# Kernel tuning notes

Hardware: AMD Instinct MI355X
Metric: run time of the kernel (lower is better)

Reference implementation:

```python
import jax, jax.numpy as jnp
import numpy as np

N_NODES = 50000
N_EDGES = 800000
D_IN = 128
D_HID = 128
NUM_LAYERS = 3
NUM_GRAPHS = 50


def setup_inputs() -> dict:
    key = jax.random.key(0)
    ks = jax.random.split(key, 8)
    x = jax.random.normal(ks[0], (N_NODES, D_IN), dtype=jnp.float32)
    edge_index = jax.random.randint(ks[1], (2, N_EDGES), 0, N_NODES, dtype=jnp.int32)
    batch = jnp.sort(jax.random.randint(ks[2], (N_NODES,), 0, NUM_GRAPHS, dtype=jnp.int32))
    # glorot-ish init for GCN weights and fc weights
    scale = 1.0 / np.sqrt(D_HID)
    Wc = jax.random.normal(ks[3], (NUM_LAYERS, D_IN, D_HID), dtype=jnp.float32) * scale
    bc = jnp.zeros((NUM_LAYERS, D_HID), dtype=jnp.float32)
    Wf = jax.random.normal(ks[4], (NUM_LAYERS, D_HID, D_HID), dtype=jnp.float32) * scale
    bf = jnp.zeros((NUM_LAYERS, D_HID), dtype=jnp.float32)
    return {"x": x, "edge_index": edge_index, "batch": batch,
            "Wc": Wc, "bc": bc, "Wf": Wf, "bf": bf}


def _gcn_forward(x, Wc, bc, Wf, bf, src, dst, deg_inv_sqrt, batch):
    norm = deg_inv_sqrt[src] * deg_inv_sqrt[dst]  # [E+N]
    for i in range(NUM_LAYERS):
        h = x @ Wc[i]                              # [N, D_HID] linear transform
        msg = h[src] * norm[:, None]               # gather + normalize, [E+N, D_HID]
        x = jax.ops.segment_sum(msg, dst, num_segments=N_NODES) + bc[i]
        x = jax.nn.relu(x)
    x = jax.ops.segment_sum(x, batch, num_segments=NUM_GRAPHS)  # global_add_pool
    for i in range(NUM_LAYERS):
        x = jax.nn.relu(x @ Wf[i] + bf[i])
    return x  # [NUM_GRAPHS, D_HID]


def reference(x, edge_index, batch, Wc, bc, Wf, bf):
    # add self-loops (PyG GCNConv default) and compute symmetric normalization
    loops = jnp.arange(N_NODES, dtype=edge_index.dtype)
    src = jnp.concatenate([edge_index[0], loops])
    dst = jnp.concatenate([edge_index[1], loops])
    deg = jax.ops.segment_sum(jnp.ones_like(dst, dtype=x.dtype), dst,
                              num_segments=N_NODES)
    deg_inv_sqrt = jnp.where(deg > 0, jax.lax.rsqrt(jnp.maximum(deg, 1.0)), 0.0)
    return _gcn_forward(x, Wc, bc, Wf, bf, src, dst, deg_inv_sqrt, batch)
```

## Files before the change

kernel.cpp:

```cpp
#include <hip/hip_runtime.h>

#define N_NODES 50000
#define N_EDGES 800000
#define D 128
#define NGRAPH 50

typedef unsigned int uint32;
typedef unsigned short u16;
typedef __attribute__((ext_vector_type(8))) short short8;
typedef __attribute__((ext_vector_type(4))) float f32x4;

__device__ inline float bf_lo(uint32 u) { union { uint32 u; float f; } c; c.u = u << 16; return c.f; }
__device__ inline float bf_hi(uint32 u) { union { uint32 u; float f; } c; c.u = u & 0xffff0000u; return c.f; }
__device__ inline u16 f2bf(float f) {
  union { float f; uint32 u; } c; c.f = f;
  uint32 r = (c.u + 0x7fffu + ((c.u >> 16) & 1u)) >> 16;
  return (u16)r;
}

__global__ void k_init(int* __restrict__ deg, const float* __restrict__ Wc,
                       u16* __restrict__ WT, const int* __restrict__ batch,
                       int* __restrict__ gstart) {
  int i = blockIdx.x * 256 + threadIdx.x;
  if (i < N_NODES) deg[i] = 0;
  if (i < 3 * 128 * 128) {
    int layer = i >> 14, rem = i & 16383;
    int n = rem >> 7, k = rem & 127;
    WT[i] = f2bf(Wc[layer * 16384 + k * 128 + n]);
  }
  if (i <= NGRAPH) {
    int lo = 0, hi = N_NODES;
    while (lo < hi) {
      int mid = (lo + hi) >> 1;
      if (batch[mid] < i) lo = mid + 1; else hi = mid;
    }
    gstart[i] = lo;
  }
}

__global__ void k_degfill(const int* __restrict__ src, const int* __restrict__ dst,
                          int* __restrict__ deg, u16* __restrict__ csr) {
  int e = blockIdx.x * 256 + threadIdx.x;
  if (e < N_EDGES) {
    int d = dst[e];
    int r = atomicAdd(&deg[d], 1);
    csr[(d << 6) + r] = (u16)src[e];
  }
}

template <int AF32>
__global__ __launch_bounds__(256) void k_gemm(const void* __restrict__ Ap,
                                              const u16* __restrict__ WT,
                                              const int* __restrict__ deg,
                                              u16* __restrict__ G) {
  __shared__ u16 so[4][16][136];
  int t = threadIdx.x;
  int wave = t >> 6, l = t & 63;
  int cl = l & 15, kgrp = l >> 4;
  int r0 = blockIdx.x * 64 + wave * 16;
  int arow = r0 + cl;
  bool valid = arow < N_NODES;

  const short8* B8 = reinterpret_cast<const short8*>(WT);

  f32x4 acc[8] = {};
#pragma unroll
  for (int k0 = 0; k0 < 4; ++k0) {
    short8 a = {};
    if (valid) {
      if (AF32) {
        const float4* A4 = reinterpret_cast<const float4*>(Ap);
        float4 v0 = A4[(size_t)arow * 32 + (k0 * 4 + kgrp) * 2];
        float4 v1 = A4[(size_t)arow * 32 + (k0 * 4 + kgrp) * 2 + 1];
        a[0] = (short)f2bf(v0.x); a[1] = (short)f2bf(v0.y);
        a[2] = (short)f2bf(v0.z); a[3] = (short)f2bf(v0.w);
        a[4] = (short)f2bf(v1.x); a[5] = (short)f2bf(v1.y);
        a[6] = (short)f2bf(v1.z); a[7] = (short)f2bf(v1.w);
      } else {
        a = reinterpret_cast<const short8*>(Ap)[(size_t)arow * 16 + k0 * 4 + kgrp];
      }
    }
#pragma unroll
    for (int c = 0; c < 8; ++c) {
      short8 b = B8[(c * 16 + cl) * 16 + k0 * 4 + kgrp];
      acc[c] = __builtin_amdgcn_mfma_f32_16x16x32_bf16(a, b, acc[c], 0, 0, 0);
    }
  }

  int rloc = kgrp * 4;
  float dj[4];
#pragma unroll
  for (int j = 0; j < 4; ++j) {
    int rr = r0 + rloc + j;
    dj[j] = (rr < N_NODES) ? rsqrtf((float)deg[rr] + 1.0f) : 0.f;
  }
#pragma unroll
  for (int c = 0; c < 8; ++c) {
#pragma unroll
    for (int j = 0; j < 4; ++j) {
      so[wave][rloc + j][c * 16 + cl] = f2bf(dj[j] * acc[c][j]);
    }
  }
#pragma unroll
  for (int i = 0; i < 4; ++i) {
    int idx = i * 64 + l;
    int rr = idx >> 4, ch = idx & 15;
    int grow = r0 + rr;
    if (grow < N_NODES) {
      *reinterpret_cast<uint4*>(&(((u16*)G)[(size_t)grow * 128 + ch * 8])) =
          *reinterpret_cast<const uint4*>(&so[wave][rr][ch * 8]);
    }
  }
}

template <int OUT_BF16>
__global__ __launch_bounds__(256) void k_agg(const uint2* __restrict__ g2,
                                             const int* __restrict__ deg,
                                             const u16* __restrict__ csr,
                                             const float* __restrict__ bc,
                                             void* __restrict__ xo) {
  int w = threadIdx.x >> 6;
  int i = blockIdx.x * 4 + w;
  if (i >= N_NODES) return;
  int l = threadIdx.x & 63;
  int half = l >> 5, c = l & 31;

  int cnt = deg[i];
  float di = rsqrtf((float)cnt + 1.0f);

  float a0 = 0.f, a1 = 0.f, a2 = 0.f, a3 = 0.f;
  if (half == 0) {
    uint2 su = g2[(size_t)i * 32 + c];
    a0 = bf_lo(su.x); a1 = bf_hi(su.x); a2 = bf_lo(su.y); a3 = bf_hi(su.y);
  }

  int myidx = (l < cnt) ? (int)csr[(i << 6) + l] : 0;
  int npair = cnt >> 1;
  int j = 0;
  for (; j + 4 <= npair; j += 4) {
    int s0 = __shfl(myidx, 2 * j + half);
    int s1 = __shfl(myidx, 2 * (j + 1) + half);
    int s2 = __shfl(myidx, 2 * (j + 2) + half);
    int s3 = __shfl(myidx, 2 * (j + 3) + half);
    uint2 u0 = g2[(size_t)s0 * 32 + c];
    uint2 u1 = g2[(size_t)s1 * 32 + c];
    uint2 u2 = g2[(size_t)s2 * 32 + c];
    uint2 u3 = g2[(size_t)s3 * 32 + c];
    a0 += bf_lo(u0.x); a1 += bf_hi(u0.x); a2 += bf_lo(u0.y); a3 += bf_hi(u0.y);
    a0 += bf_lo(u1.x); a1 += bf_hi(u1.x); a2 += bf_lo(u1.y); a3 += bf_hi(u1.y);
    a0 += bf_lo(u2.x); a1 += bf_hi(u2.x); a2 += bf_lo(u2.y); a3 += bf_hi(u2.y);
    a0 += bf_lo(u3.x); a1 += bf_hi(u3.x); a2 += bf_lo(u3.y); a3 += bf_hi(u3.y);
  }
  for (; j < npair; ++j) {
    int s = __shfl(myidx, 2 * j + half);
    uint2 u = g2[(size_t)s * 32 + c];
    a0 += bf_lo(u.x); a1 += bf_hi(u.x); a2 += bf_lo(u.y); a3 += bf_hi(u.y);
  }
  if (cnt & 1) {
    int s = __shfl(myidx, cnt - 1);
    if (half == 0) {
      uint2 u = g2[(size_t)s * 32 + c];
      a0 += bf_lo(u.x); a1 += bf_hi(u.x); a2 += bf_lo(u.y); a3 += bf_hi(u.y);
    }
  }
  a0 += __shfl_xor(a0, 32);
  a1 += __shfl_xor(a1, 32);
  a2 += __shfl_xor(a2, 32);
  a3 += __shfl_xor(a3, 32);

  if (half == 0) {
    float4 bb = reinterpret_cast<const float4*>(bc)[c];
    float r0 = fmaxf(fmaf(di, a0, bb.x), 0.f);
    float r1 = fmaxf(fmaf(di, a1, bb.y), 0.f);
    float r2 = fmaxf(fmaf(di, a2, bb.z), 0.f);
    float r3 = fmaxf(fmaf(di, a3, bb.w), 0.f);
    if (OUT_BF16) {
      ushort4 o;
      o.x = f2bf(r0); o.y = f2bf(r1); o.z = f2bf(r2); o.w = f2bf(r3);
      reinterpret_cast<ushort4*>(xo)[(size_t)i * 32 + c] = o;
    } else {
      reinterpret_cast<float4*>(xo)[(size_t)i * 32 + c] = make_float4(r0, r1, r2, r3);
    }
  }
}

__global__ __launch_bounds__(256) void k_pool(const float* __restrict__ x,
                                              const int* __restrict__ gstart,
                                              float* __restrict__ pp) {
  __shared__ float2 red[4][64];
  int g = blockIdx.x, ch = blockIdx.y;
  int s = gstart[g], e = gstart[g + 1];
  long len = e - s;
  int cs = s + (int)(len * ch / 8);
  int ce = s + (int)(len * (ch + 1) / 8);
  int sub = threadIdx.x >> 6, l = threadIdx.x & 63;
  const float2* x2 = reinterpret_cast<const float2*>(x);
  float2 acc = make_float2(0.f, 0.f);
  for (int n = cs + sub; n < ce; n += 4) {
    float2 v = x2[(size_t)n * 64 + l];
    acc.x += v.x;
    acc.y += v.y;
  }
  red[sub][l] = acc;
  __syncthreads();
  if (sub == 0) {
    float2 a = red[0][l];
    a.x += red[1][l].x + red[2][l].x + red[3][l].x;
    a.y += red[1][l].y + red[2][l].y + red[3][l].y;
    pp[(ch * NGRAPH + g) * D + 2 * l] = a.x;
    pp[(ch * NGRAPH + g) * D + 2 * l + 1] = a.y;
  }
}

__global__ __launch_bounds__(128) void k_fc(const float* __restrict__ pp,
                                            const float* __restrict__ Wf,
                                            const float* __restrict__ bf,
                                            float* __restrict__ out) {
  __shared__ float row[D];
  int g = blockIdx.x, c = threadIdx.x;
  float v = 0.f;
#pragma unroll
  for (int ch = 0; ch < 8; ++ch) v += pp[(ch * NGRAPH + g) * D + c];
  row[c] = v;
  __syncthreads();
  for (int l = 0; l < 3; ++l) {
    const float* W = Wf + l * D * D;
    float s = bf[l * D + c];
    for (int k = 0; k < D; ++k) s = fmaf(row[k], W[k * D + c], s);
    s = fmaxf(s, 0.f);
    __syncthreads();
    row[c] = s;
    __syncthreads();
  }
  out[g * D + c] = row[c];
}

extern "C" void kernel_launch(void* const* d_in, const int* in_sizes, int n_in,
                              void* d_out, int out_size, void* d_ws, size_t ws_size,
                              hipStream_t stream) {
  const float* x   = (const float*)d_in[0];
  const int*   ei  = (const int*)d_in[1];
  const int* batch = (const int*)d_in[2];
  const float* Wc  = (const float*)d_in[3];
  const float* bc  = (const float*)d_in[4];
  const float* Wf  = (const float*)d_in[5];
  const float* bf  = (const float*)d_in[6];
  float* out = (float*)d_out;
  const int* src = ei;
  const int* dst = ei + N_EDGES;

  char* ws = (char*)d_ws;
  size_t o = 0;
  auto take = [&](size_t b) -> void* {
    void* p = ws + o;
    o = (o + b + 255) & ~(size_t)255;
    return p;
  };
  int*  deg    = (int*)take(N_NODES * 4);
  int*  gstart = (int*)take(64 * 4);
  u16*  WT     = (u16*)take((size_t)3 * D * D * 2);
  u16*  csr    = (u16*)take((size_t)N_NODES * 64 * 2);
  u16*  xb     = (u16*)take((size_t)N_NODES * D * 2);
  u16*  gbuf   = (u16*)take((size_t)N_NODES * D * 2);
  float* xbuf  = (float*)take((size_t)N_NODES * D * 4);
  float* pp    = (float*)take((size_t)8 * NGRAPH * D * 4);
  (void)ws_size; (void)in_sizes; (void)n_in; (void)out_size;

  const int NB = (N_NODES + 255) / 256;
  k_init<<<NB, 256, 0, stream>>>(deg, Wc, WT, batch, gstart);
  k_degfill<<<(N_EDGES + 255) / 256, 256, 0, stream>>>(src, dst, deg, csr);

  const int GB = (N_NODES + 63) / 64;
  const int AB = (N_NODES + 3) / 4;
  k_gemm<1><<<GB, 256, 0, stream>>>(x, WT + 0 * D * D, deg, gbuf);
  k_agg<1><<<AB, 256, 0, stream>>>((const uint2*)gbuf, deg, csr, bc + 0 * D, xb);
  k_gemm<0><<<GB, 256, 0, stream>>>(xb, WT + 1 * D * D, deg, gbuf);
  k_agg<1><<<AB, 256, 0, stream>>>((const uint2*)gbuf, deg, csr, bc + 1 * D, xb);
  k_gemm<0><<<GB, 256, 0, stream>>>(xb, WT + 2 * D * D, deg, gbuf);
  k_agg<0><<<AB, 256, 0, stream>>>((const uint2*)gbuf, deg, csr, bc + 2 * D, xbuf);

  k_pool<<<dim3(NGRAPH, 8), 256, 0, stream>>>(xbuf, gstart, pp);
  k_fc<<<NGRAPH, 128, 0, stream>>>(pp, Wf, bf, out);
}
```

Baseline: 250.5 us.

## Widen aggregation gathers to 16-byte rows and partition degree fill by destination

```diff
diff --git a/kernel.cpp b/kernel.cpp
--- a/kernel.cpp
+++ b/kernel.cpp
@@ -40,11 +40,14 @@
 
 __global__ void k_degfill(const int* __restrict__ src, const int* __restrict__ dst,
                           int* __restrict__ deg, u16* __restrict__ csr) {
-  int e = blockIdx.x * 256 + threadIdx.x;
+  int part = blockIdx.x & 7;
+  int e = (blockIdx.x >> 3) * 256 + threadIdx.x;
   if (e < N_EDGES) {
     int d = dst[e];
-    int r = atomicAdd(&deg[d], 1);
-    csr[(d << 6) + r] = (u16)src[e];
+    if (d / 6250 == part) {
+      int r = atomicAdd(&deg[d], 1);
+      csr[(d << 6) + r] = (u16)src[e];
+    }
   }
 }
 
@@ -113,8 +116,12 @@
   }
 }
 
+#define ACCUM(u) do { \
+    a0 += bf_lo((u).x); a1 += bf_hi((u).x); a2 += bf_lo((u).y); a3 += bf_hi((u).y); \
+    a4 += bf_lo((u).z); a5 += bf_hi((u).z); a6 += bf_lo((u).w); a7 += bf_hi((u).w); } while (0)
+
 template <int OUT_BF16>
-__global__ __launch_bounds__(256) void k_agg(const uint2* __restrict__ g2,
+__global__ __launch_bounds__(256) void k_agg(const uint4* __restrict__ g4,
                                              const int* __restrict__ deg,
                                              const u16* __restrict__ csr,
                                              const float* __restrict__ bc,
@@ -123,63 +130,76 @@
   int i = blockIdx.x * 4 + w;
   if (i >= N_NODES) return;
   int l = threadIdx.x & 63;
-  int half = l >> 5, c = l & 31;
+  int q = l >> 4, c = l & 15;
 
   int cnt = deg[i];
   float di = rsqrtf((float)cnt + 1.0f);
 
   float a0 = 0.f, a1 = 0.f, a2 = 0.f, a3 = 0.f;
-  if (half == 0) {
-    uint2 su = g2[(size_t)i * 32 + c];
-    a0 = bf_lo(su.x); a1 = bf_hi(su.x); a2 = bf_lo(su.y); a3 = bf_hi(su.y);
+  float a4 = 0.f, a5 = 0.f, a6 = 0.f, a7 = 0.f;
+  if (q == 0) {
+    uint4 su = g4[(size_t)i * 16 + c];
+    ACCUM(su);
   }
 
   int myidx = (l < cnt) ? (int)csr[(i << 6) + l] : 0;
-  int npair = cnt >> 1;
+
+  int nq = cnt >> 2;
   int j = 0;
-  for (; j + 4 <= npair; j += 4) {
-    int s0 = __shfl(myidx, 2 * j + half);
-    int s1 = __shfl(myidx, 2 * (j + 1) + half);
-    int s2 = __shfl(myidx, 2 * (j + 2) + half);
-    int s3 = __shfl(myidx, 2 * (j + 3) + half);
-    uint2 u0 = g2[(size_t)s0 * 32 + c];
-    uint2 u1 = g2[(size_t)s1 * 32 + c];
-    uint2 u2 = g2[(size_t)s2 * 32 + c];
-    uint2 u3 = g2[(size_t)s3 * 32 + c];
-    a0 += bf_lo(u0.x); a1 += bf_hi(u0.x); a2 += bf_lo(u0.y); a3 += bf_hi(u0.y);
-    a0 += bf_lo(u1.x); a1 += bf_hi(u1.x); a2 += bf_lo(u1.y); a3 += bf_hi(u1.y);
-    a0 += bf_lo(u2.x); a1 += bf_hi(u2.x); a2 += bf_lo(u2.y); a3 += bf_hi(u2.y);
-    a0 += bf_lo(u3.x); a1 += bf_hi(u3.x); a2 += bf_lo(u3.y); a3 += bf_hi(u3.y);
-  }
-  for (; j < npair; ++j) {
-    int s = __shfl(myidx, 2 * j + half);
-    uint2 u = g2[(size_t)s * 32 + c];
-    a0 += bf_lo(u.x); a1 += bf_hi(u.x); a2 += bf_lo(u.y); a3 += bf_hi(u.y);
-  }
-  if (cnt & 1) {
-    int s = __shfl(myidx, cnt - 1);
-    if (half == 0) {
-      uint2 u = g2[(size_t)s * 32 + c];
-      a0 += bf_lo(u.x); a1 += bf_hi(u.x); a2 += bf_lo(u.y); a3 += bf_hi(u.y);
-    }
-  }
-  a0 += __shfl_xor(a0, 32);
-  a1 += __shfl_xor(a1, 32);
-  a2 += __shfl_xor(a2, 32);
-  a3 += __shfl_xor(a3, 32);
-
-  if (half == 0) {
-    float4 bb = reinterpret_cast<const float4*>(bc)[c];
-    float r0 = fmaxf(fmaf(di, a0, bb.x), 0.f);
-    float r1 = fmaxf(fmaf(di, a1, bb.y), 0.f);
-    float r2 = fmaxf(fmaf(di, a2, bb.z), 0.f);
-    float r3 = fmaxf(fmaf(di, a3, bb.w), 0.f);
+  for (; j + 4 <= nq; j += 4) {
+    int s0 = __shfl(myidx, 4 * j + q);
+    int s1 = __shfl(myidx, 4 * j + 4 + q);
+    int s2 = __shfl(myidx, 4 * j + 8 + q);
+    int s3 = __shfl(myidx, 4 * j + 12 + q);
+    uint4 u0 = g4[(size_t)s0 * 16 + c];
+    uint4 u1 = g4[(size_t)s1 * 16 + c];
+    uint4 u2 = g4[(size_t)s2 * 16 + c];
+    uint4 u3 = g4[(size_t)s3 * 16 + c];
+    ACCUM(u0); ACCUM(u1); ACCUM(u2); ACCUM(u3);
+  }
+  for (; j < nq; ++j) {
+    int s = __shfl(myidx, 4 * j + q);
+    uint4 u = g4[(size_t)s * 16 + c];
+    ACCUM(u);
+  }
+  if (cnt & 3) {
+    int idx = 4 * nq + q;
+    int s = __shfl(myidx, idx < cnt ? idx : 0);
+    if (idx < cnt) {
+      uint4 u = g4[(size_t)s * 16 + c];
+      ACCUM(u);
+    }
+  }
+  a0 += __shfl_xor(a0, 16); a0 += __shfl_xor(a0, 32);
+  a1 += __shfl_xor(a1, 16); a1 += __shfl_xor(a1, 32);
+  a2 += __shfl_xor(a2, 16); a2 += __shfl_xor(a2, 32);
+  a3 += __shfl_xor(a3, 16); a3 += __shfl_xor(a3, 32);
+  a4 += __shfl_xor(a4, 16); a4 += __shfl_xor(a4, 32);
+  a5 += __shfl_xor(a5, 16); a5 += __shfl_xor(a5, 32);
+  a6 += __shfl_xor(a6, 16); a6 += __shfl_xor(a6, 32);
+  a7 += __shfl_xor(a7, 16); a7 += __shfl_xor(a7, 32);
+
+  if (q == 0) {
+    float4 b0 = reinterpret_cast<const float4*>(bc)[c * 2];
+    float4 b1 = reinterpret_cast<const float4*>(bc)[c * 2 + 1];
+    float r0 = fmaxf(fmaf(di, a0, b0.x), 0.f);
+    float r1 = fmaxf(fmaf(di, a1, b0.y), 0.f);
+    float r2 = fmaxf(fmaf(di, a2, b0.z), 0.f);
+    float r3 = fmaxf(fmaf(di, a3, b0.w), 0.f);
+    float r4 = fmaxf(fmaf(di, a4, b1.x), 0.f);
+    float r5 = fmaxf(fmaf(di, a5, b1.y), 0.f);
+    float r6 = fmaxf(fmaf(di, a6, b1.z), 0.f);
+    float r7 = fmaxf(fmaf(di, a7, b1.w), 0.f);
     if (OUT_BF16) {
-      ushort4 o;
-      o.x = f2bf(r0); o.y = f2bf(r1); o.z = f2bf(r2); o.w = f2bf(r3);
-      reinterpret_cast<ushort4*>(xo)[(size_t)i * 32 + c] = o;
+      uint4 o;
+      o.x = ((uint32)f2bf(r1) << 16) | f2bf(r0);
+      o.y = ((uint32)f2bf(r3) << 16) | f2bf(r2);
+      o.z = ((uint32)f2bf(r5) << 16) | f2bf(r4);
+      o.w = ((uint32)f2bf(r7) << 16) | f2bf(r6);
+      reinterpret_cast<uint4*>(xo)[(size_t)i * 16 + c] = o;
     } else {
-      reinterpret_cast<float4*>(xo)[(size_t)i * 32 + c] = make_float4(r0, r1, r2, r3);
+      reinterpret_cast<float4*>(xo)[(size_t)i * 32 + c * 2] = make_float4(r0, r1, r2, r3);
+      reinterpret_cast<float4*>(xo)[(size_t)i * 32 + c * 2 + 1] = make_float4(r4, r5, r6, r7);
     }
   }
 }
@@ -268,16 +288,16 @@
 
   const int NB = (N_NODES + 255) / 256;
   k_init<<<NB, 256, 0, stream>>>(deg, Wc, WT, batch, gstart);
-  k_degfill<<<(N_EDGES + 255) / 256, 256, 0, stream>>>(src, dst, deg, csr);
+  k_degfill<<<8 * ((N_EDGES + 255) / 256), 256, 0, stream>>>(src, dst, deg, csr);
 
   const int GB = (N_NODES + 63) / 64;
   const int AB = (N_NODES + 3) / 4;
   k_gemm<1><<<GB, 256, 0, stream>>>(x, WT + 0 * D * D, deg, gbuf);
-  k_agg<1><<<AB, 256, 0, stream>>>((const uint2*)gbuf, deg, csr, bc + 0 * D, xb);
+  k_agg<1><<<AB, 256, 0, stream>>>((const uint4*)gbuf, deg, csr, bc + 0 * D, xb);
   k_gemm<0><<<GB, 256, 0, stream>>>(xb, WT + 1 * D * D, deg, gbuf);
-  k_agg<1><<<AB, 256, 0, stream>>>((const uint2*)gbuf, deg, csr, bc + 1 * D, xb);
+  k_agg<1><<<AB, 256, 0, stream>>>((const uint4*)gbuf, deg, csr, bc + 1 * D, xb);
   k_gemm<0><<<GB, 256, 0, stream>>>(xb, WT + 2 * D * D, deg, gbuf);
-  k_agg<0><<<AB, 256, 0, stream>>>((const uint2*)gbuf, deg, csr, bc + 2 * D, xbuf);
+  k_agg<0><<<AB, 256, 0, stream>>>((const uint4*)gbuf, deg, csr, bc + 2 * D, xbuf);
 
   k_pool<<<dim3(NGRAPH, 8), 256, 0, stream>>>(xbuf, gstart, pp);
   k_fc<<<NGRAPH, 128, 0, stream>>>(pp, Wf, bf, out);
```

Result: faster. 231.7 us (-7.5%).
